# Performance work log

Measured on AMD Instinct MI355X. Metric: run time of the kernel, lower is better.

The kernel has to match this reference:

```python
import jax, jax.numpy as jnp
import numpy as np


def hard_sigmoid(v):
    # Keras 1.x default LSTM inner activation
    return jnp.clip(0.2 * v + 0.5, 0.0, 1.0)


def lstm_step(h, c, x_t, W, U, b):
    # Keras gate order: i, f, c(candidate), o
    z = x_t @ W + h @ U + b
    i, f, g, o = jnp.split(z, 4, axis=-1)
    i = hard_sigmoid(i)
    f = hard_sigmoid(f)
    g = jnp.tanh(g)
    o = hard_sigmoid(o)
    c_new = f * c + i * g
    h_new = o * jnp.tanh(c_new)
    return h_new, c_new


def setup_inputs() -> dict:
    key = jax.random.key(0)
    ks = jax.random.split(key, 8)
    B, L, D = 64, 1024, 512
    s = 0.05
    w = lambda k, shape: jax.random.normal(k, shape, jnp.float32) * s
    return {
        "x": jax.random.normal(ks[0], (B, L, D), jnp.float32),
        "Wr": w(ks[1], (D, 4 * D)),
        "Ur": w(ks[2], (D, 4 * D)),
        "br": jnp.zeros((4 * D,), jnp.float32),
        "Ww": w(ks[3], (D, 4 * D)),
        "Uw": w(ks[4], (D, 4 * D)),
        "bw": jnp.zeros((4 * D,), jnp.float32),
        "Wc": w(ks[5], (2 * D, D)),
        "bc": jnp.zeros((D,), jnp.float32),
    }


def reference(x, Wr, Ur, br, Ww, Uw, bw, Wc, bc):
    B, L, D = x.shape
    z0 = jnp.zeros((B, D), x.dtype)

    # --- reader LSTM over the full sequence (equation 1): o (L, B, D) ---
    def r_step(carry, x_t):
        h, c = carry
        h, c = lstm_step(h, c, x_t, Wr, Ur, br)
        return (h, c), h

    _, o_seq = jax.lax.scan(r_step, (z0, z0), jnp.swapaxes(x, 0, 1))

    # --- compose-and-write recurrence over memory (equations 2-6) ---
    mem0 = x  # mem_0 = input_to_read

    def w_step(carry, o_t):
        mem, hw, cw = carry                                   # mem: (B, L, D)
        z = jax.nn.softmax(jnp.einsum('bd,bld->bl', o_t, mem))  # attention over memory
        m_rt = jnp.einsum('bl,bld->bd', z, mem)                 # weighted read
        c_t = jnp.concatenate([o_t, m_rt], axis=-1) @ Wc + bc   # composer (linear)
        hw, cw = lstm_step(hw, cw, c_t, Ww, Uw, bw)             # writer LSTM step
        mem = mem * (1.0 - z[..., None]) + hw[:, None, :] * z[..., None]
        return (mem, hw, cw), None

    (mem_T, h_T, _), _ = jax.lax.scan(w_step, (mem0, z0, z0), o_seq)
    # return_mode == 'last_output'
    return h_T
```

## Files before the change

### kernel.cpp

```cpp
#include <hip/hip_runtime.h>
#include <math.h>

#define Bb 64
#define Ll 1024
#define Dd 512
#define G4 2048
#define KK 8
#define PART_STRIDE 524
#define WSL 12
#define RSL 8

__device__ __forceinline__ float hsig(float v){ return fminf(fmaxf(0.2f*v + 0.5f, 0.f), 1.f); }

__global__ __launch_bounds__(256) void wf_build(const float* __restrict__ Wc, const float* __restrict__ Ww,
                                                const float* __restrict__ Uw, float* __restrict__ Wf){
    const int k0 = (blockIdx.x >> 3) * 16;
    const int j  = (blockIdx.x & 7) * 256 + threadIdx.x;
    if (k0 < 2 * Dd){
        float acc[16];
        #pragma unroll
        for (int kk = 0; kk < 16; ++kk) acc[kk] = 0.f;
        for (int m = 0; m < Dd; ++m){
            float wv = Ww[(size_t)m * G4 + j];
            #pragma unroll
            for (int kk = 0; kk < 16; ++kk)
                acc[kk] = fmaf(Wc[(size_t)(k0 + kk) * Dd + m], wv, acc[kk]);
        }
        #pragma unroll
        for (int kk = 0; kk < 16; ++kk) Wf[(size_t)(k0 + kk) * G4 + j] = acc[kk];
    } else {
        #pragma unroll
        for (int kk = 0; kk < 16; ++kk)
            Wf[(size_t)(k0 + kk) * G4 + j] = Uw[(size_t)(k0 + kk - 2 * Dd) * G4 + j];
    }
}

__global__ __launch_bounds__(256) void bf_build(const float* __restrict__ bc, const float* __restrict__ Ww,
                                                const float* __restrict__ bw, float* __restrict__ bf){
    int j = blockIdx.x * 256 + threadIdx.x;
    float s = bw[j];
    for (int m = 0; m < Dd; ++m) s = fmaf(bc[m], Ww[(size_t)m * G4 + j], s);
    bf[j] = s;
}

__global__ __launch_bounds__(256) void gemm_reader(const float* __restrict__ xt, const float* __restrict__ h,
                                                   const float* __restrict__ Wr, const float* __restrict__ Ur,
                                                   float* __restrict__ part){
    __shared__ float inT[64][65];
    __shared__ float wT[64][32];
    const int bx = blockIdx.x;
    const int jt = bx & 63, ks = bx >> 6;
    const int j0 = jt * 32;
    const int k0 = ks * 256;
    const int tid = threadIdx.x;
    const int tj4 = (tid & 7) * 4;
    const int tb  = tid >> 3;
    float a00=0.f,a01=0.f,a02=0.f,a03=0.f;
    float a10=0.f,a11=0.f,a12=0.f,a13=0.f;
    for (int kk = 0; kk < 256; kk += 64){
        #pragma unroll
        for (int i = 0; i < 16; ++i){
            int idx = tid + i * 256;
            int b = idx >> 6, k = idx & 63;
            int kg = k0 + kk + k;
            inT[b][k] = (kg < Dd) ? xt[(size_t)b * (Ll * Dd) + kg] : h[b * Dd + kg - Dd];
        }
        #pragma unroll
        for (int i = 0; i < 8; ++i){
            int idx = tid + i * 256;
            int k = idx >> 5, j = idx & 31;
            int kg = k0 + kk + k;
            wT[k][j] = (kg < Dd) ? Wr[(size_t)kg * G4 + j0 + j] : Ur[(size_t)(kg - Dd) * G4 + j0 + j];
        }
        __syncthreads();
        #pragma unroll 8
        for (int k = 0; k < 64; ++k){
            float4 wv = *(const float4*)&wT[k][tj4];
            float i0 = inT[tb][k];
            float i1 = inT[tb + 32][k];
            a00 = fmaf(i0, wv.x, a00); a01 = fmaf(i0, wv.y, a01);
            a02 = fmaf(i0, wv.z, a02); a03 = fmaf(i0, wv.w, a03);
            a10 = fmaf(i1, wv.x, a10); a11 = fmaf(i1, wv.y, a11);
            a12 = fmaf(i1, wv.z, a12); a13 = fmaf(i1, wv.w, a13);
        }
        __syncthreads();
    }
    size_t o0 = (size_t)(ks * Bb + tb) * G4 + j0 + tj4;
    size_t o1 = (size_t)(ks * Bb + tb + 32) * G4 + j0 + tj4;
    *(float4*)&part[o0] = make_float4(a00, a01, a02, a03);
    *(float4*)&part[o1] = make_float4(a10, a11, a12, a13);
}

__global__ __launch_bounds__(256) void reader_pw(const float* __restrict__ part, const float* __restrict__ br,
                                                 float* __restrict__ h, float* __restrict__ c){
    int idx = blockIdx.x * 256 + threadIdx.x;
    int b = idx >> 9, d = idx & 511;
    float z[4];
    #pragma unroll
    for (int g = 0; g < 4; ++g){
        int j = g * Dd + d;
        float s = br[j];
        #pragma unroll
        for (int ks = 0; ks < 4; ++ks) s += part[(size_t)(ks * Bb + b) * G4 + j];
        z[g] = s;
    }
    float i = hsig(z[0]), f = hsig(z[1]), g2 = tanhf(z[2]), o = hsig(z[3]);
    float cn = fmaf(f, c[idx], i * g2);
    c[idx] = cn;
    h[idx] = o * tanhf(cn);
}

__global__ __launch_bounds__(256) void gemm_fast(const float* __restrict__ o, const float* __restrict__ mrt,
                                                 const float* __restrict__ hw, const float* __restrict__ Wf,
                                                 float* __restrict__ partW,
                                                 const float* __restrict__ xt1, const float* __restrict__ Wr,
                                                 const float* __restrict__ Ur, float* __restrict__ partR){
    __shared__ float inT[2][64][68];
    __shared__ float wT[2][64][36];
    const int bxg = blockIdx.x;
    const bool writer = (bxg < WSL * 64);
    const int bx = writer ? bxg : bxg - WSL * 64;
    const int jt = bx & 63;
    const int ks = bx >> 6;
    const int j0 = jt * 32;
    const int k0 = ks * 128;
    const int tid = threadIdx.x;
    const int tj4 = (tid & 7) * 4;
    const int tb  = tid >> 3;

    float4 aR0, aR1, aR2, aR3, wR0, wR1;
    auto LOAD = [&](int kk){
        #pragma unroll
        for (int i = 0; i < 4; ++i){
            int lin = tid + i * 256;
            int b = lin >> 4, k4 = (lin & 15) * 4;
            int kg = k0 + kk + k4;
            const float* src;
            if (writer){
                if (kg < Dd)           src = o   + b * Dd + kg;
                else if (kg < 2 * Dd)  src = mrt + b * Dd + kg - Dd;
                else                   src = hw  + b * Dd + kg - 2 * Dd;
            } else {
                src = (kg < Dd) ? xt1 + (size_t)b * (Ll * Dd) + kg
                                : o + b * Dd + kg - Dd;
            }
            float4 v = *(const float4*)src;
            if (i == 0) aR0 = v; else if (i == 1) aR1 = v; else if (i == 2) aR2 = v; else aR3 = v;
        }
        #pragma unroll
        for (int i = 0; i < 2; ++i){
            int lin = tid + i * 256;
            int k = lin >> 3, j4 = (lin & 7) * 4;
            int kg = k0 + kk + k;
            const float* src;
            if (writer) src = Wf + (size_t)kg * G4 + j0 + j4;
            else        src = (kg < Dd) ? Wr + (size_t)kg * G4 + j0 + j4
                                        : Ur + (size_t)(kg - Dd) * G4 + j0 + j4;
            float4 v = *(const float4*)src;
            if (i == 0) wR0 = v; else wR1 = v;
        }
    };
    auto STORE = [&](int buf){
        #pragma unroll
        for (int i = 0; i < 4; ++i){
            int lin = tid + i * 256;
            int b = lin >> 4, k4 = (lin & 15) * 4;
            float4 v = (i == 0) ? aR0 : (i == 1) ? aR1 : (i == 2) ? aR2 : aR3;
            *(float4*)&inT[buf][b][k4] = v;
        }
        #pragma unroll
        for (int i = 0; i < 2; ++i){
            int lin = tid + i * 256;
            int k = lin >> 3, j4 = (lin & 7) * 4;
            float4 v = (i == 0) ? wR0 : wR1;
            *(float4*)&wT[buf][k][j4] = v;
        }
    };

    float a00=0.f,a01=0.f,a02=0.f,a03=0.f;
    float a10=0.f,a11=0.f,a12=0.f,a13=0.f;

    LOAD(0);
    STORE(0);
    __syncthreads();
    LOAD(64);
    #pragma unroll 8
    for (int k = 0; k < 64; ++k){
        float4 wv = *(const float4*)&wT[0][k][tj4];
        float i0 = inT[0][tb][k];
        float i1 = inT[0][tb + 32][k];
        a00 = fmaf(i0, wv.x, a00); a01 = fmaf(i0, wv.y, a01);
        a02 = fmaf(i0, wv.z, a02); a03 = fmaf(i0, wv.w, a03);
        a10 = fmaf(i1, wv.x, a10); a11 = fmaf(i1, wv.y, a11);
        a12 = fmaf(i1, wv.z, a12); a13 = fmaf(i1, wv.w, a13);
    }
    STORE(1);
    __syncthreads();
    #pragma unroll 8
    for (int k = 0; k < 64; ++k){
        float4 wv = *(const float4*)&wT[1][k][tj4];
        float i0 = inT[1][tb][k];
        float i1 = inT[1][tb + 32][k];
        a00 = fmaf(i0, wv.x, a00); a01 = fmaf(i0, wv.y, a01);
        a02 = fmaf(i0, wv.z, a02); a03 = fmaf(i0, wv.w, a03);
        a10 = fmaf(i1, wv.x, a10); a11 = fmaf(i1, wv.y, a11);
        a12 = fmaf(i1, wv.z, a12); a13 = fmaf(i1, wv.w, a13);
    }
    float* part = writer ? partW : partR;
    size_t o0 = (size_t)(ks * Bb + tb) * G4 + j0 + tj4;
    size_t o1 = (size_t)(ks * Bb + tb + 32) * G4 + j0 + tj4;
    *(float4*)&part[o0] = make_float4(a00, a01, a02, a03);
    *(float4*)&part[o1] = make_float4(a10, a11, a12, a13);
}

__global__ __launch_bounds__(256) void pw_both(const float* __restrict__ partW, const float* __restrict__ bfv,
                                               float* __restrict__ hw, float* __restrict__ cw,
                                               float* __restrict__ out, int last,
                                               const float* __restrict__ partR, const float* __restrict__ br,
                                               float* __restrict__ h, float* __restrict__ c){
    const int bxg = blockIdx.x;
    const int writer = (bxg < 128) ? 1 : 0;
    const int idx = (writer ? bxg : bxg - 128) * 256 + threadIdx.x;
    const int b = idx >> 9, d = idx & 511;
    float z[4];
    #pragma unroll
    for (int g = 0; g < 4; ++g){
        int j = g * Dd + d;
        float s;
        if (writer){
            s = bfv[j];
            #pragma unroll
            for (int sl = 0; sl < WSL; ++sl) s += partW[(size_t)(sl * Bb + b) * G4 + j];
        } else {
            s = br[j];
            #pragma unroll
            for (int sl = 0; sl < RSL; ++sl) s += partR[(size_t)(sl * Bb + b) * G4 + j];
        }
        z[g] = s;
    }
    float i = hsig(z[0]), f = hsig(z[1]), g2 = tanhf(z[2]), o = hsig(z[3]);
    if (writer){
        float cn = fmaf(f, cw[idx], i * g2);
        cw[idx] = cn;
        float hn = o * tanhf(cn);
        hw[idx] = hn;
        if (last) out[idx] = hn;
    } else {
        float cn = fmaf(f, c[idx], i * g2);
        c[idx] = cn;
        h[idx] = o * tanhf(cn);
    }
}

__global__ __launch_bounds__(256, 4) void mega3(const float* memB, float* memOut,
                                                const float* __restrict__ o,
                                                float* __restrict__ scores, const float* __restrict__ Mb,
                                                const float* __restrict__ Sinv,
                                                float* __restrict__ part,
                                                float* __restrict__ Dv, float* __restrict__ Cv,
                                                const float* __restrict__ hwring,
                                                int mode, int p){
    __shared__ float DL[64];
    __shared__ float CORRL[64];
    __shared__ float CL[64][KK];
    __shared__ float GL[KK];
    __shared__ float HWL[KK][Dd];
    const int bid = blockIdx.x;
    const int b = bid >> 4, lb = bid & 15;
    const int tid = threadIdx.x;
    const int lane = tid & 63;
    const int wvi = tid >> 6;
    const int gw = lb * 4 + wvi;
    const int d0 = lane * 4, d1 = 256 + lane * 4;

    if (mode == 2){
        for (int ii = wvi; ii < p; ii += 4){
            const float* ov = o + b * Dd + lane * 8;
            const float* hv = hwring + ((size_t)ii * Bb + b) * Dd + lane * 8;
            float4 x0 = *(const float4*)ov;
            float4 x1 = *(const float4*)(ov + 4);
            float4 y0 = *(const float4*)hv;
            float4 y1 = *(const float4*)(hv + 4);
            float s = x0.x*y0.x + x0.y*y0.y + x0.z*y0.z + x0.w*y0.w
                    + x1.x*y1.x + x1.y*y1.y + x1.z*y1.z + x1.w*y1.w;
            #pragma unroll
            for (int off = 32; off; off >>= 1) s += __shfl_xor(s, off);
            if (lane == 0) GL[ii] = s;
        }
        __syncthreads();
    }

    if (mode){
        if (tid < 64){
            const int l = lb * 64 + tid;
            const size_t cbase = (size_t)(b * Ll + l) * KK;
            float z = __expf(scores[b * Ll + l] - Mb[b]) * Sinv[b];
            float om = 1.f - z;
            const int pm1 = (mode == 1) ? (KK - 1) : (p - 1);
            float cl[KK];
            float Dn;
            if (pm1 == 0){
                Dn = om;
                #pragma unroll
                for (int i = 0; i < KK; ++i) cl[i] = 0.f;
            } else {
                Dn = Dv[b * Ll + l] * om;
                #pragma unroll
                for (int i = 0; i < KK; ++i) cl[i] = Cv[cbase + i] * om;
                #pragma unroll
                for (int i = 0; i < KK; ++i) if (i > pm1) cl[i] = 0.f;
            }
            cl[pm1] = z;
            DL[tid] = Dn;
            #pragma unroll
            for (int i = 0; i < KK; ++i) CL[tid][i] = cl[i];
            if (mode == 2){
                Dv[b * Ll + l] = Dn;
                #pragma unroll
                for (int i = 0; i < KK; ++i) Cv[cbase + i] = cl[i];
                float corr = 0.f;
                #pragma unroll
                for (int i = 0; i < KK; ++i) corr = fmaf(cl[i], (i < p) ? GL[i] : 0.f, corr);
                CORRL[tid] = corr;
            }
        }
        if (mode == 1){
            for (int i = tid; i < KK * Dd; i += 256){
                int s = i >> 9, d = i & 511;
                HWL[s][d] = hwring[((size_t)s * Bb + b) * Dd + d];
            }
        }
        __syncthreads();
    }

    float4 oa  = *(const float4*)(o + b * Dd + d0);
    float4 obv = *(const float4*)(o + b * Dd + d1);
    const int lbase = gw * 16;
    float* srow = scores + b * Ll;

    float mA = -INFINITY, sAs = 0.f, mB = -INFINITY, sBs = 0.f;
    float A0x=0.f,A0y=0.f,A0z=0.f,A0w=0.f, A1x=0.f,A1y=0.f,A1z=0.f,A1w=0.f;
    float B0x=0.f,B0y=0.f,B0z=0.f,B0w=0.f, B1x=0.f,B1y=0.f,B1z=0.f,B1w=0.f;
    float my_s = 0.f;
    size_t baseA = ((size_t)b * Ll + lbase) * Dd;
    size_t baseB = baseA + (size_t)8 * Dd;

    if (mode == 1){
        #pragma unroll 2
        for (int r = 0; r < 8; ++r){
            const int locA = wvi * 16 + r, locB = locA + 8;
            float4 vA0 = *(const float4*)(memB + baseA + d0);
            float4 vA1 = *(const float4*)(memB + baseA + d1);
            float4 vB0 = *(const float4*)(memB + baseB + d0);
            float4 vB1 = *(const float4*)(memB + baseB + d1);
            float DnA = DL[locA], DnB = DL[locB];
            vA0.x *= DnA; vA0.y *= DnA; vA0.z *= DnA; vA0.w *= DnA;
            vA1.x *= DnA; vA1.y *= DnA; vA1.z *= DnA; vA1.w *= DnA;
            vB0.x *= DnB; vB0.y *= DnB; vB0.z *= DnB; vB0.w *= DnB;
            vB1.x *= DnB; vB1.y *= DnB; vB1.z *= DnB; vB1.w *= DnB;
            #pragma unroll
            for (int i = 0; i < KK; ++i){
                float cA = CL[locA][i], cB = CL[locB][i];
                float4 h0 = *(const float4*)&HWL[i][d0];
                float4 h1 = *(const float4*)&HWL[i][d1];
                vA0.x = fmaf(cA, h0.x, vA0.x); vA0.y = fmaf(cA, h0.y, vA0.y);
                vA0.z = fmaf(cA, h0.z, vA0.z); vA0.w = fmaf(cA, h0.w, vA0.w);
                vA1.x = fmaf(cA, h1.x, vA1.x); vA1.y = fmaf(cA, h1.y, vA1.y);
                vA1.z = fmaf(cA, h1.z, vA1.z); vA1.w = fmaf(cA, h1.w, vA1.w);
                vB0.x = fmaf(cB, h0.x, vB0.x); vB0.y = fmaf(cB, h0.y, vB0.y);
                vB0.z = fmaf(cB, h0.z, vB0.z); vB0.w = fmaf(cB, h0.w, vB0.w);
                vB1.x = fmaf(cB, h1.x, vB1.x); vB1.y = fmaf(cB, h1.y, vB1.y);
                vB1.z = fmaf(cB, h1.z, vB1.z); vB1.w = fmaf(cB, h1.w, vB1.w);
            }
            *(float4*)(memOut + baseA + d0) = vA0;
            *(float4*)(memOut + baseA + d1) = vA1;
            *(float4*)(memOut + baseB + d0) = vB0;
            *(float4*)(memOut + baseB + d1) = vB1;
            float sa = vA0.x*oa.x + vA0.y*oa.y + vA0.z*oa.z + vA0.w*oa.w
                     + vA1.x*obv.x + vA1.y*obv.y + vA1.z*obv.z + vA1.w*obv.w;
            float sb = vB0.x*oa.x + vB0.y*oa.y + vB0.z*oa.z + vB0.w*oa.w
                     + vB1.x*obv.x + vB1.y*obv.y + vB1.z*obv.z + vB1.w*obv.w;
            #pragma unroll
            for (int off = 32; off; off >>= 1){
                sa += __shfl_xor(sa, off);
                sb += __shfl_xor(sb, off);
            }
            if (lane == 0){ srow[lbase + r] = sa; srow[lbase + 8 + r] = sb; }
            float nmA = fmaxf(mA, sa);
            float scA = __expf(mA - nmA);
            float wtA = __expf(sa - nmA);
            sAs = fmaf(sAs, scA, wtA);
            A0x = fmaf(A0x, scA, vA0.x * wtA); A0y = fmaf(A0y, scA, vA0.y * wtA);
            A0z = fmaf(A0z, scA, vA0.z * wtA); A0w = fmaf(A0w, scA, vA0.w * wtA);
            A1x = fmaf(A1x, scA, vA1.x * wtA); A1y = fmaf(A1y, scA, vA1.y * wtA);
            A1z = fmaf(A1z, scA, vA1.z * wtA); A1w = fmaf(A1w, scA, vA1.w * wtA);
            mA = nmA;
            float nmB = fmaxf(mB, sb);
            float scB = __expf(mB - nmB);
            float wtB = __expf(sb - nmB);
            sBs = fmaf(sBs, scB, wtB);
            B0x = fmaf(B0x, scB, vB0.x * wtB); B0y = fmaf(B0y, scB, vB0.y * wtB);
            B0z = fmaf(B0z, scB, vB0.z * wtB); B0w = fmaf(B0w, scB, vB0.w * wtB);
            B1x = fmaf(B1x, scB, vB1.x * wtB); B1y = fmaf(B1y, scB, vB1.y * wtB);
            B1z = fmaf(B1z, scB, vB1.z * wtB); B1w = fmaf(B1w, scB, vB1.w * wtB);
            mB = nmB;
            baseA += Dd; baseB += Dd;
        }
    } else {
        #pragma unroll 2
        for (int r = 0; r < 8; ++r){
            const int locA = wvi * 16 + r, locB = locA + 8;
            float4 vA0 = *(const float4*)(memB + baseA + d0);
            float4 vA1 = *(const float4*)(memB + baseA + d1);
            float4 vB0 = *(const float4*)(memB + baseB + d0);
            float4 vB1 = *(const float4*)(memB + baseB + d1);
            float sa = vA0.x*oa.x + vA0.y*oa.y + vA0.z*oa.z + vA0.w*oa.w
                     + vA1.x*obv.x + vA1.y*obv.y + vA1.z*obv.z + vA1.w*obv.w;
            float sb = vB0.x*oa.x + vB0.y*oa.y + vB0.z*oa.z + vB0.w*oa.w
                     + vB1.x*obv.x + vB1.y*obv.y + vB1.z*obv.z + vB1.w*obv.w;
            #pragma unroll
            for (int off = 32; off; off >>= 1){
                sa += __shfl_xor(sa, off);
                sb += __shfl_xor(sb, off);
            }
            float DnA = 1.f, DnB = 1.f;
            if (mode == 2){
                DnA = DL[locA]; DnB = DL[locB];
                sa = fmaf(DnA, sa, CORRL[locA]);
                sb = fmaf(DnB, sb, CORRL[locB]);
            }
            if (lane == 0){ srow[lbase + r] = sa; srow[lbase + 8 + r] = sb; }
            if (lane == r)     my_s = sa;
            if (lane == 8 + r) my_s = sb;
            float nmA = fmaxf(mA, sa);
            float scA = __expf(mA - nmA);
            float wtA = __expf(sa - nmA);
            float wdA = wtA * DnA;
            sAs = fmaf(sAs, scA, wtA);
            A0x = fmaf(A0x, scA, vA0.x * wdA); A0y = fmaf(A0y, scA, vA0.y * wdA);
            A0z = fmaf(A0z, scA, vA0.z * wdA); A0w = fmaf(A0w, scA, vA0.w * wdA);
            A1x = fmaf(A1x, scA, vA1.x * wdA); A1y = fmaf(A1y, scA, vA1.y * wdA);
            A1z = fmaf(A1z, scA, vA1.z * wdA); A1w = fmaf(A1w, scA, vA1.w * wdA);
            mA = nmA;
            float nmB = fmaxf(mB, sb);
            float scB = __expf(mB - nmB);
            float wtB = __expf(sb - nmB);
            float wdB = wtB * DnB;
            sBs = fmaf(sBs, scB, wtB);
            B0x = fmaf(B0x, scB, vB0.x * wdB); B0y = fmaf(B0y, scB, vB0.y * wdB);
            B0z = fmaf(B0z, scB, vB0.z * wdB); B0w = fmaf(B0w, scB, vB0.w * wdB);
            B1x = fmaf(B1x, scB, vB1.x * wdB); B1y = fmaf(B1y, scB, vB1.y * wdB);
            B1z = fmaf(B1z, scB, vB1.z * wdB); B1w = fmaf(B1w, scB, vB1.w * wdB);
            mB = nmB;
            baseA += Dd; baseB += Dd;
        }
    }
    float M = fmaxf(mA, mB);
    float eA = __expf(mA - M), eB = __expf(mB - M);
    float ssum = sAs * eA + sBs * eB;
    float* pp = part + (size_t)(b * 64 + gw) * PART_STRIDE;
    *(float4*)(pp + d0) = make_float4(A0x * eA + B0x * eB, A0y * eA + B0y * eB,
                                      A0z * eA + B0z * eB, A0w * eA + B0w * eB);
    *(float4*)(pp + d1) = make_float4(A1x * eA + B1x * eB, A1y * eA + B1y * eB,
                                      A1z * eA + B1z * eB, A1w * eA + B1w * eB);
    if (lane == 0){ pp[512] = M; pp[513] = ssum; }
    if (mode == 2){
        float wexp = (lane < 16) ? __expf(my_s - M) : 0.f;
        float gacc = 0.f;
        const int ci = lane & 7;
        #pragma unroll
        for (int l = 0; l < 16; ++l){
            float wl = __shfl(wexp, l);
            gacc = fmaf(wl, CL[wvi * 16 + l][ci], gacc);
        }
        if (lane < 8) pp[514 + lane] = gacc;
    }
}

__global__ __launch_bounds__(256) void small_a(const float* __restrict__ part, float* __restrict__ mrt,
                                               float* __restrict__ Mb, float* __restrict__ Sinv,
                                               const float* __restrict__ hwring, int p){
    const int b = blockIdx.x >> 2, dseg = blockIdx.x & 3;
    const int tid = threadIdx.x;
    __shared__ float ews[64];
    __shared__ float psum[256];
    __shared__ float gam[KK][8];
    if (tid < 64){
        const float* pp = part + (size_t)(b * 64 + tid) * PART_STRIDE;
        float mw = pp[512], sw = pp[513];
        float M = mw;
        #pragma unroll
        for (int off = 32; off; off >>= 1) M = fmaxf(M, __shfl_xor(M, off));
        float e = __expf(mw - M);
        float Ssum = sw * e;
        #pragma unroll
        for (int off = 32; off; off >>= 1) Ssum += __shfl_xor(Ssum, off);
        float Si = 1.f / Ssum;
        ews[tid] = e * Si;
        if (dseg == 0 && tid == 0){ Mb[b] = M; Sinv[b] = Si; }
    }
    __syncthreads();
    if (p > 0 && tid < 64){
        const int i = tid & 7, ch = tid >> 3;
        float s = 0.f;
        #pragma unroll
        for (int w2 = 0; w2 < 8; ++w2)
            s = fmaf(part[(size_t)(b * 64 + ch * 8 + w2) * PART_STRIDE + 514 + i], ews[ch * 8 + w2], s);
        gam[i][ch] = s;
    }
    __syncthreads();
    if (p > 0 && tid < 8){
        float s = gam[tid][0];
        #pragma unroll
        for (int ch = 1; ch < 8; ++ch) s += gam[tid][ch];
        gam[tid][0] = s;
    }
    const int dl = tid & 127, half = tid >> 7;
    const int d = dseg * 128 + dl;
    const float* pb = part + (size_t)(b * 64 + half * 32) * PART_STRIDE + d;
    float s = 0.f;
    #pragma unroll 8
    for (int w2 = 0; w2 < 32; ++w2)
        s = fmaf(pb[(size_t)w2 * PART_STRIDE], ews[half * 32 + w2], s);
    psum[tid] = s;
    __syncthreads();
    if (half == 0){
        float r = psum[tid] + psum[tid + 128];
        for (int i = 0; i < p; ++i)
            r = fmaf(gam[i][0], hwring[((size_t)i * Bb + b) * Dd + d], r);
        mrt[b * Dd + d] = r;
    }
}

extern "C" void kernel_launch(void* const* d_in, const int* in_sizes, int n_in,
                              void* d_out, int out_size, void* d_ws, size_t ws_size,
                              hipStream_t stream) {
    (void)in_sizes; (void)n_in; (void)out_size;
    const float* x  = (const float*)d_in[0];
    const float* Wr = (const float*)d_in[1];
    const float* Ur = (const float*)d_in[2];
    const float* br = (const float*)d_in[3];
    const float* Ww = (const float*)d_in[4];
    const float* Uw = (const float*)d_in[5];
    const float* bw = (const float*)d_in[6];
    const float* Wc = (const float*)d_in[7];
    const float* bc = (const float*)d_in[8];
    float* out = (float*)d_out;

    float* w = (float*)d_ws;
    float* mem     = w; w += (size_t)Bb * Ll * Dd;
    float* scores  = w; w += (size_t)Bb * Ll;
    float* part_me = w; w += (size_t)Bb * 64 * PART_STRIDE;
    float* Mb      = w; w += 64;
    float* Sinv    = w; w += 64;
    float* mrt     = w; w += (size_t)Bb * Dd;
    float* Dv      = w; w += (size_t)Bb * Ll;
    float* Cv      = w; w += (size_t)Bb * Ll * KK;
    float* h_r     = w; w += (size_t)Bb * Dd;
    float* c_r     = w; w += (size_t)Bb * Dd;
    float* cw      = w; w += (size_t)Bb * Dd;
    float* hwring  = w; w += (size_t)KK * Bb * Dd;
    float* partR   = w; w += (size_t)RSL * Bb * G4;
    float* partW   = w; w += (size_t)WSL * Bb * G4;
    float* Wf      = w; w += (size_t)1536 * G4;
    float* bf      = w; w += G4;
    size_t need = (size_t)(w - (float*)d_ws) * sizeof(float);
    if (ws_size < need) return;

    hipMemsetAsync(h_r, 0, (size_t)(3 + KK) * Bb * Dd * sizeof(float), stream);
    wf_build<<<(1536 / 16) * 8, 256, 0, stream>>>(Wc, Ww, Uw, Wf);
    bf_build<<<G4 / 256, 256, 0, stream>>>(bc, Ww, bw, bf);

    gemm_reader<<<256, 256, 0, stream>>>(x, h_r, Wr, Ur, partR);
    reader_pw<<<128, 256, 0, stream>>>(partR, br, h_r, c_r);

    for (int t = 0; t < Ll; ++t){
        const int p = t & (KK - 1);
        const int mode = (t == 0) ? 0 : ((p == 0) ? 1 : 2);
        const float* mi = (t <= KK) ? x : mem;
        mega3<<<1024, 256, 0, stream>>>(mi, mem, h_r, scores, Mb, Sinv, part_me,
                                        Dv, Cv, hwring, mode, p);
        small_a<<<256, 256, 0, stream>>>(part_me, mrt, Mb, Sinv, hwring, (mode == 2) ? p : 0);
        int tn = (t + 1 < Ll) ? t + 1 : t;
        const float* hwprev = hwring + ((size_t)((t + KK - 1) & (KK - 1)) * Bb) * Dd;
        gemm_fast<<<(WSL + RSL) * 64, 256, 0, stream>>>(h_r, mrt, hwprev, Wf, partW,
                                                        x + (size_t)tn * Dd, Wr, Ur, partR);
        float* hwnew = hwring + ((size_t)(t & (KK - 1)) * Bb) * Dd;
        pw_both<<<256, 256, 0, stream>>>(partW, bf, hwnew, cw, out, t == Ll - 1 ? 1 : 0,
                                         partR, br, h_r, c_r);
    }
}
```

Measured before the change: 68.69 ms.

## Double lazy memory-update window and split attention kernel into factor and materialize variants

Raises the deferred low-rank memory update window from 8 to 16 steps, so the full memory tensor is rewritten half as often. The monolithic attention kernel becomes two specialised kernels: one that materialises the memory update and one that works from the factored form, which removes mode branches and the large shared hw buffer from the common path. The trade-off is more correction coefficients per row, larger Cv/part buffers, and a 32 KB shared tile in the materialising kernel, which may lower occupancy there.

```diff
diff --git a/kernel.cpp b/kernel.cpp
--- a/kernel.cpp
+++ b/kernel.cpp
@@ -5,8 +5,8 @@
 #define Ll 1024
 #define Dd 512
 #define G4 2048
-#define KK 8
-#define PART_STRIDE 524
+#define KK 16
+#define PART_STRIDE 532
 #define WSL 12
 #define RSL 8
 
@@ -252,19 +252,18 @@
     }
 }
 
-__global__ __launch_bounds__(256, 4) void mega3(const float* memB, float* memOut,
-                                                const float* __restrict__ o,
-                                                float* __restrict__ scores, const float* __restrict__ Mb,
-                                                const float* __restrict__ Sinv,
-                                                float* __restrict__ part,
-                                                float* __restrict__ Dv, float* __restrict__ Cv,
-                                                const float* __restrict__ hwring,
-                                                int mode, int p){
+__global__ __launch_bounds__(256, 4) void mega_factor(const float* __restrict__ memB,
+                                                      const float* __restrict__ o,
+                                                      float* __restrict__ scores, const float* __restrict__ Mb,
+                                                      const float* __restrict__ Sinv,
+                                                      float* __restrict__ part,
+                                                      float* __restrict__ Dv, float* __restrict__ Cv,
+                                                      const float* __restrict__ hwring,
+                                                      int mode, int p){
     __shared__ float DL[64];
     __shared__ float CORRL[64];
     __shared__ float CL[64][KK];
     __shared__ float GL[KK];
-    __shared__ float HWL[KK][Dd];
     const int bid = blockIdx.x;
     const int b = bid >> 4, lb = bid & 15;
     const int tid = threadIdx.x;
@@ -288,15 +287,13 @@
             if (lane == 0) GL[ii] = s;
         }
         __syncthreads();
-    }
-
-    if (mode){
+
         if (tid < 64){
             const int l = lb * 64 + tid;
             const size_t cbase = (size_t)(b * Ll + l) * KK;
             float z = __expf(scores[b * Ll + l] - Mb[b]) * Sinv[b];
             float om = 1.f - z;
-            const int pm1 = (mode == 1) ? (KK - 1) : (p - 1);
+            const int pm1 = p - 1;
             float cl[KK];
             float Dn;
             if (pm1 == 0){
@@ -314,21 +311,13 @@
             DL[tid] = Dn;
             #pragma unroll
             for (int i = 0; i < KK; ++i) CL[tid][i] = cl[i];
-            if (mode == 2){
-                Dv[b * Ll + l] = Dn;
-                #pragma unroll
-                for (int i = 0; i < KK; ++i) Cv[cbase + i] = cl[i];
-                float corr = 0.f;
-                #pragma unroll
-                for (int i = 0; i < KK; ++i) corr = fmaf(cl[i], (i < p) ? GL[i] : 0.f, corr);
-                CORRL[tid] = corr;
-            }
-        }
-        if (mode == 1){
-            for (int i = tid; i < KK * Dd; i += 256){
-                int s = i >> 9, d = i & 511;
-                HWL[s][d] = hwring[((size_t)s * Bb + b) * Dd + d];
-            }
+            Dv[b * Ll + l] = Dn;
+            #pragma unroll
+            for (int i = 0; i < KK; ++i) Cv[cbase + i] = cl[i];
+            float corr = 0.f;
+            #pragma unroll
+            for (int i = 0; i < KK; ++i) corr = fmaf(cl[i], (i < p) ? GL[i] : 0.f, corr);
+            CORRL[tid] = corr;
         }
         __syncthreads();
     }
@@ -345,115 +334,52 @@
     size_t baseA = ((size_t)b * Ll + lbase) * Dd;
     size_t baseB = baseA + (size_t)8 * Dd;
 
-    if (mode == 1){
-        #pragma unroll 2
-        for (int r = 0; r < 8; ++r){
-            const int locA = wvi * 16 + r, locB = locA + 8;
-            float4 vA0 = *(const float4*)(memB + baseA + d0);
-            float4 vA1 = *(const float4*)(memB + baseA + d1);
-            float4 vB0 = *(const float4*)(memB + baseB + d0);
-            float4 vB1 = *(const float4*)(memB + baseB + d1);
-            float DnA = DL[locA], DnB = DL[locB];
-            vA0.x *= DnA; vA0.y *= DnA; vA0.z *= DnA; vA0.w *= DnA;
-            vA1.x *= DnA; vA1.y *= DnA; vA1.z *= DnA; vA1.w *= DnA;
-            vB0.x *= DnB; vB0.y *= DnB; vB0.z *= DnB; vB0.w *= DnB;
-            vB1.x *= DnB; vB1.y *= DnB; vB1.z *= DnB; vB1.w *= DnB;
-            #pragma unroll
-            for (int i = 0; i < KK; ++i){
-                float cA = CL[locA][i], cB = CL[locB][i];
-                float4 h0 = *(const float4*)&HWL[i][d0];
-                float4 h1 = *(const float4*)&HWL[i][d1];
-                vA0.x = fmaf(cA, h0.x, vA0.x); vA0.y = fmaf(cA, h0.y, vA0.y);
-                vA0.z = fmaf(cA, h0.z, vA0.z); vA0.w = fmaf(cA, h0.w, vA0.w);
-                vA1.x = fmaf(cA, h1.x, vA1.x); vA1.y = fmaf(cA, h1.y, vA1.y);
-                vA1.z = fmaf(cA, h1.z, vA1.z); vA1.w = fmaf(cA, h1.w, vA1.w);
-                vB0.x = fmaf(cB, h0.x, vB0.x); vB0.y = fmaf(cB, h0.y, vB0.y);
-                vB0.z = fmaf(cB, h0.z, vB0.z); vB0.w = fmaf(cB, h0.w, vB0.w);
-                vB1.x = fmaf(cB, h1.x, vB1.x); vB1.y = fmaf(cB, h1.y, vB1.y);
-                vB1.z = fmaf(cB, h1.z, vB1.z); vB1.w = fmaf(cB, h1.w, vB1.w);
-            }
-            *(float4*)(memOut + baseA + d0) = vA0;
-            *(float4*)(memOut + baseA + d1) = vA1;
-            *(float4*)(memOut + baseB + d0) = vB0;
-            *(float4*)(memOut + baseB + d1) = vB1;
-            float sa = vA0.x*oa.x + vA0.y*oa.y + vA0.z*oa.z + vA0.w*oa.w
-                     + vA1.x*obv.x + vA1.y*obv.y + vA1.z*obv.z + vA1.w*obv.w;
-            float sb = vB0.x*oa.x + vB0.y*oa.y + vB0.z*oa.z + vB0.w*oa.w
-                     + vB1.x*obv.x + vB1.y*obv.y + vB1.z*obv.z + vB1.w*obv.w;
-            #pragma unroll
-            for (int off = 32; off; off >>= 1){
-                sa += __shfl_xor(sa, off);
-                sb += __shfl_xor(sb, off);
-            }
-            if (lane == 0){ srow[lbase + r] = sa; srow[lbase + 8 + r] = sb; }
-            float nmA = fmaxf(mA, sa);
-            float scA = __expf(mA - nmA);
-            float wtA = __expf(sa - nmA);
-            sAs = fmaf(sAs, scA, wtA);
-            A0x = fmaf(A0x, scA, vA0.x * wtA); A0y = fmaf(A0y, scA, vA0.y * wtA);
-            A0z = fmaf(A0z, scA, vA0.z * wtA); A0w = fmaf(A0w, scA, vA0.w * wtA);
-            A1x = fmaf(A1x, scA, vA1.x * wtA); A1y = fmaf(A1y, scA, vA1.y * wtA);
-            A1z = fmaf(A1z, scA, vA1.z * wtA); A1w = fmaf(A1w, scA, vA1.w * wtA);
-            mA = nmA;
-            float nmB = fmaxf(mB, sb);
-            float scB = __expf(mB - nmB);
-            float wtB = __expf(sb - nmB);
-            sBs = fmaf(sBs, scB, wtB);
-            B0x = fmaf(B0x, scB, vB0.x * wtB); B0y = fmaf(B0y, scB, vB0.y * wtB);
-            B0z = fmaf(B0z, scB, vB0.z * wtB); B0w = fmaf(B0w, scB, vB0.w * wtB);
-            B1x = fmaf(B1x, scB, vB1.x * wtB); B1y = fmaf(B1y, scB, vB1.y * wtB);
-            B1z = fmaf(B1z, scB, vB1.z * wtB); B1w = fmaf(B1w, scB, vB1.w * wtB);
-            mB = nmB;
-            baseA += Dd; baseB += Dd;
-        }
-    } else {
-        #pragma unroll 2
-        for (int r = 0; r < 8; ++r){
-            const int locA = wvi * 16 + r, locB = locA + 8;
-            float4 vA0 = *(const float4*)(memB + baseA + d0);
-            float4 vA1 = *(const float4*)(memB + baseA + d1);
-            float4 vB0 = *(const float4*)(memB + baseB + d0);
-            float4 vB1 = *(const float4*)(memB + baseB + d1);
-            float sa = vA0.x*oa.x + vA0.y*oa.y + vA0.z*oa.z + vA0.w*oa.w
-                     + vA1.x*obv.x + vA1.y*obv.y + vA1.z*obv.z + vA1.w*obv.w;
-            float sb = vB0.x*oa.x + vB0.y*oa.y + vB0.z*oa.z + vB0.w*oa.w
-                     + vB1.x*obv.x + vB1.y*obv.y + vB1.z*obv.z + vB1.w*obv.w;
-            #pragma unroll
-            for (int off = 32; off; off >>= 1){
-                sa += __shfl_xor(sa, off);
-                sb += __shfl_xor(sb, off);
-            }
-            float DnA = 1.f, DnB = 1.f;
-            if (mode == 2){
-                DnA = DL[locA]; DnB = DL[locB];
-                sa = fmaf(DnA, sa, CORRL[locA]);
-                sb = fmaf(DnB, sb, CORRL[locB]);
-            }
-            if (lane == 0){ srow[lbase + r] = sa; srow[lbase + 8 + r] = sb; }
-            if (lane == r)     my_s = sa;
-            if (lane == 8 + r) my_s = sb;
-            float nmA = fmaxf(mA, sa);
-            float scA = __expf(mA - nmA);
-            float wtA = __expf(sa - nmA);
-            float wdA = wtA * DnA;
-            sAs = fmaf(sAs, scA, wtA);
-            A0x = fmaf(A0x, scA, vA0.x * wdA); A0y = fmaf(A0y, scA, vA0.y * wdA);
-            A0z = fmaf(A0z, scA, vA0.z * wdA); A0w = fmaf(A0w, scA, vA0.w * wdA);
-            A1x = fmaf(A1x, scA, vA1.x * wdA); A1y = fmaf(A1y, scA, vA1.y * wdA);
-            A1z = fmaf(A1z, scA, vA1.z * wdA); A1w = fmaf(A1w, scA, vA1.w * wdA);
-            mA = nmA;
-            float nmB = fmaxf(mB, sb);
-            float scB = __expf(mB - nmB);
-            float wtB = __expf(sb - nmB);
-            float wdB = wtB * DnB;
-            sBs = fmaf(sBs, scB, wtB);
-            B0x = fmaf(B0x, scB, vB0.x * wdB); B0y = fmaf(B0y, scB, vB0.y * wdB);
-            B0z = fmaf(B0z, scB, vB0.z * wdB); B0w = fmaf(B0w, scB, vB0.w * wdB);
-            B1x = fmaf(B1x, scB, vB1.x * wdB); B1y = fmaf(B1y, scB, vB1.y * wdB);
-            B1z = fmaf(B1z, scB, vB1.z * wdB); B1w = fmaf(B1w, scB, vB1.w * wdB);
-            mB = nmB;
-            baseA += Dd; baseB += Dd;
-        }
+    #pragma unroll 2
+    for (int r = 0; r < 8; ++r){
+        const int locA = wvi * 16 + r, locB = locA + 8;
+        float4 vA0 = *(const float4*)(memB + baseA + d0);
+        float4 vA1 = *(const float4*)(memB + baseA + d1);
+        float4 vB0 = *(const float4*)(memB + baseB + d0);
+        float4 vB1 = *(const float4*)(memB + baseB + d1);
+        float sa = vA0.x*oa.x + vA0.y*oa.y + vA0.z*oa.z + vA0.w*oa.w
+                 + vA1.x*obv.x + vA1.y*obv.y + vA1.z*obv.z + vA1.w*obv.w;
+        float sb = vB0.x*oa.x + vB0.y*oa.y + vB0.z*oa.z + vB0.w*oa.w
+                 + vB1.x*obv.x + vB1.y*obv.y + vB1.z*obv.z + vB1.w*obv.w;
+        #pragma unroll
+        for (int off = 32; off; off >>= 1){
+            sa += __shfl_xor(sa, off);
+            sb += __shfl_xor(sb, off);
+        }
+        float DnA = 1.f, DnB = 1.f;
+        if (mode == 2){
+            DnA = DL[locA]; DnB = DL[locB];
+            sa = fmaf(DnA, sa, CORRL[locA]);
+            sb = fmaf(DnB, sb, CORRL[locB]);
+        }
+        if (lane == 0){ srow[lbase + r] = sa; srow[lbase + 8 + r] = sb; }
+        if (lane == r)     my_s = sa;
+        if (lane == 8 + r) my_s = sb;
+        float nmA = fmaxf(mA, sa);
+        float scA = __expf(mA - nmA);
+        float wtA = __expf(sa - nmA);
+        float wdA = wtA * DnA;
+        sAs = fmaf(sAs, scA, wtA);
+        A0x = fmaf(A0x, scA, vA0.x * wdA); A0y = fmaf(A0y, scA, vA0.y * wdA);
+        A0z = fmaf(A0z, scA, vA0.z * wdA); A0w = fmaf(A0w, scA, vA0.w * wdA);
+        A1x = fmaf(A1x, scA, vA1.x * wdA); A1y = fmaf(A1y, scA, vA1.y * wdA);
+        A1z = fmaf(A1z, scA, vA1.z * wdA); A1w = fmaf(A1w, scA, vA1.w * wdA);
+        mA = nmA;
+        float nmB = fmaxf(mB, sb);
+        float scB = __expf(mB - nmB);
+        float wtB = __expf(sb - nmB);
+        float wdB = wtB * DnB;
+        sBs = fmaf(sBs, scB, wtB);
+        B0x = fmaf(B0x, scB, vB0.x * wdB); B0y = fmaf(B0y, scB, vB0.y * wdB);
+        B0z = fmaf(B0z, scB, vB0.z * wdB); B0w = fmaf(B0w, scB, vB0.w * wdB);
+        B1x = fmaf(B1x, scB, vB1.x * wdB); B1y = fmaf(B1y, scB, vB1.y * wdB);
+        B1z = fmaf(B1z, scB, vB1.z * wdB); B1w = fmaf(B1w, scB, vB1.w * wdB);
+        mB = nmB;
+        baseA += Dd; baseB += Dd;
     }
     float M = fmaxf(mA, mB);
     float eA = __expf(mA - M), eB = __expf(mB - M);
@@ -467,14 +393,134 @@
     if (mode == 2){
         float wexp = (lane < 16) ? __expf(my_s - M) : 0.f;
         float gacc = 0.f;
-        const int ci = lane & 7;
+        const int ci = lane & 15;
         #pragma unroll
         for (int l = 0; l < 16; ++l){
             float wl = __shfl(wexp, l);
             gacc = fmaf(wl, CL[wvi * 16 + l][ci], gacc);
         }
-        if (lane < 8) pp[514 + lane] = gacc;
-    }
+        if (lane < 16) pp[514 + lane] = gacc;
+    }
+}
+
+__global__ __launch_bounds__(256, 4) void mega_mat(const float* __restrict__ memB, float* __restrict__ memOut,
+                                                   const float* __restrict__ o,
+                                                   float* __restrict__ scores, const float* __restrict__ Mb,
+                                                   const float* __restrict__ Sinv,
+                                                   float* __restrict__ part,
+                                                   const float* __restrict__ Dv, const float* __restrict__ Cv,
+                                                   const float* __restrict__ hwring){
+    __shared__ float DL[64];
+    __shared__ float CL[64][KK];
+    __shared__ float HWL[KK][Dd];
+    const int bid = blockIdx.x;
+    const int b = bid >> 4, lb = bid & 15;
+    const int tid = threadIdx.x;
+    const int lane = tid & 63;
+    const int wvi = tid >> 6;
+    const int gw = lb * 4 + wvi;
+    const int d0 = lane * 4, d1 = 256 + lane * 4;
+
+    if (tid < 64){
+        const int l = lb * 64 + tid;
+        const size_t cbase = (size_t)(b * Ll + l) * KK;
+        float z = __expf(scores[b * Ll + l] - Mb[b]) * Sinv[b];
+        float om = 1.f - z;
+        float cl[KK];
+        float Dn = Dv[b * Ll + l] * om;
+        #pragma unroll
+        for (int i = 0; i < KK; ++i) cl[i] = Cv[cbase + i] * om;
+        cl[KK - 1] = z;
+        DL[tid] = Dn;
+        #pragma unroll
+        for (int i = 0; i < KK; ++i) CL[tid][i] = cl[i];
+    }
+    for (int i = tid; i < KK * Dd; i += 256){
+        int s = i >> 9, d = i & 511;
+        HWL[s][d] = hwring[((size_t)s * Bb + b) * Dd + d];
+    }
+    __syncthreads();
+
+    float4 oa  = *(const float4*)(o + b * Dd + d0);
+    float4 obv = *(const float4*)(o + b * Dd + d1);
+    const int lbase = gw * 16;
+    float* srow = scores + b * Ll;
+
+    float mA = -INFINITY, sAs = 0.f, mB = -INFINITY, sBs = 0.f;
+    float A0x=0.f,A0y=0.f,A0z=0.f,A0w=0.f, A1x=0.f,A1y=0.f,A1z=0.f,A1w=0.f;
+    float B0x=0.f,B0y=0.f,B0z=0.f,B0w=0.f, B1x=0.f,B1y=0.f,B1z=0.f,B1w=0.f;
+    size_t baseA = ((size_t)b * Ll + lbase) * Dd;
+    size_t baseB = baseA + (size_t)8 * Dd;
+
+    #pragma unroll 2
+    for (int r = 0; r < 8; ++r){
+        const int locA = wvi * 16 + r, locB = locA + 8;
+        float4 vA0 = *(const float4*)(memB + baseA + d0);
+        float4 vA1 = *(const float4*)(memB + baseA + d1);
+        float4 vB0 = *(const float4*)(memB + baseB + d0);
+        float4 vB1 = *(const float4*)(memB + baseB + d1);
+        float DnA = DL[locA], DnB = DL[locB];
+        vA0.x *= DnA; vA0.y *= DnA; vA0.z *= DnA; vA0.w *= DnA;
+        vA1.x *= DnA; vA1.y *= DnA; vA1.z *= DnA; vA1.w *= DnA;
+        vB0.x *= DnB; vB0.y *= DnB; vB0.z *= DnB; vB0.w *= DnB;
+        vB1.x *= DnB; vB1.y *= DnB; vB1.z *= DnB; vB1.w *= DnB;
+        #pragma unroll
+        for (int i = 0; i < KK; ++i){
+            float cA = CL[locA][i], cB = CL[locB][i];
+            float4 h0 = *(const float4*)&HWL[i][d0];
+            float4 h1 = *(const float4*)&HWL[i][d1];
+            vA0.x = fmaf(cA, h0.x, vA0.x); vA0.y = fmaf(cA, h0.y, vA0.y);
+            vA0.z = fmaf(cA, h0.z, vA0.z); vA0.w = fmaf(cA, h0.w, vA0.w);
+            vA1.x = fmaf(cA, h1.x, vA1.x); vA1.y = fmaf(cA, h1.y, vA1.y);
+            vA1.z = fmaf(cA, h1.z, vA1.z); vA1.w = fmaf(cA, h1.w, vA1.w);
+            vB0.x = fmaf(cB, h0.x, vB0.x); vB0.y = fmaf(cB, h0.y, vB0.y);
+            vB0.z = fmaf(cB, h0.z, vB0.z); vB0.w = fmaf(cB, h0.w, vB0.w);
+            vB1.x = fmaf(cB, h1.x, vB1.x); vB1.y = fmaf(cB, h1.y, vB1.y);
+            vB1.z = fmaf(cB, h1.z, vB1.z); vB1.w = fmaf(cB, h1.w, vB1.w);
+        }
+        *(float4*)(memOut + baseA + d0) = vA0;
+        *(float4*)(memOut + baseA + d1) = vA1;
+        *(float4*)(memOut + baseB + d0) = vB0;
+        *(float4*)(memOut + baseB + d1) = vB1;
+        float sa = vA0.x*oa.x + vA0.y*oa.y + vA0.z*oa.z + vA0.w*oa.w
+                 + vA1.x*obv.x + vA1.y*obv.y + vA1.z*obv.z + vA1.w*obv.w;
+        float sb = vB0.x*oa.x + vB0.y*oa.y + vB0.z*oa.z + vB0.w*oa.w
+                 + vB1.x*obv.x + vB1.y*obv.y + vB1.z*obv.z + vB1.w*obv.w;
+        #pragma unroll
+        for (int off = 32; off; off >>= 1){
+            sa += __shfl_xor(sa, off);
+            sb += __shfl_xor(sb, off);
+        }
+        if (lane == 0){ srow[lbase + r] = sa; srow[lbase + 8 + r] = sb; }
+        float nmA = fmaxf(mA, sa);
+        float scA = __expf(mA - nmA);
+        float wtA = __expf(sa - nmA);
+        sAs = fmaf(sAs, scA, wtA);
+        A0x = fmaf(A0x, scA, vA0.x * wtA); A0y = fmaf(A0y, scA, vA0.y * wtA);
+        A0z = fmaf(A0z, scA, vA0.z * wtA); A0w = fmaf(A0w, scA, vA0.w * wtA);
+        A1x = fmaf(A1x, scA, vA1.x * wtA); A1y = fmaf(A1y, scA, vA1.y * wtA);
+        A1z = fmaf(A1z, scA, vA1.z * wtA); A1w = fmaf(A1w, scA, vA1.w * wtA);
+        mA = nmA;
+        float nmB = fmaxf(mB, sb);
+        float scB = __expf(mB - nmB);
+        float wtB = __expf(sb - nmB);
+        sBs = fmaf(sBs, scB, wtB);
+        B0x = fmaf(B0x, scB, vB0.x * wtB); B0y = fmaf(B0y, scB, vB0.y * wtB);
+        B0z = fmaf(B0z, scB, vB0.z * wtB); B0w = fmaf(B0w, scB, vB0.w * wtB);
+        B1x = fmaf(B1x, scB, vB1.x * wtB); B1y = fmaf(B1y, scB, vB1.y * wtB);
+        B1z = fmaf(B1z, scB, vB1.z * wtB); B1w = fmaf(B1w, scB, vB1.w * wtB);
+        mB = nmB;
+        baseA += Dd; baseB += Dd;
+    }
+    float M = fmaxf(mA, mB);
+    float eA = __expf(mA - M), eB = __expf(mB - M);
+    float ssum = sAs * eA + sBs * eB;
+    float* pp = part + (size_t)(b * 64 + gw) * PART_STRIDE;
+    *(float4*)(pp + d0) = make_float4(A0x * eA + B0x * eB, A0y * eA + B0y * eB,
+                                      A0z * eA + B0z * eB, A0w * eA + B0w * eB);
+    *(float4*)(pp + d1) = make_float4(A1x * eA + B1x * eB, A1y * eA + B1y * eB,
+                                      A1z * eA + B1z * eB, A1w * eA + B1w * eB);
+    if (lane == 0){ pp[512] = M; pp[513] = ssum; }
 }
 
 __global__ __launch_bounds__(256) void small_a(const float* __restrict__ part, float* __restrict__ mrt,
@@ -500,8 +546,8 @@
         if (dseg == 0 && tid == 0){ Mb[b] = M; Sinv[b] = Si; }
     }
     __syncthreads();
-    if (p > 0 && tid < 64){
-        const int i = tid & 7, ch = tid >> 3;
+    if (p > 0 && tid < 128){
+        const int i = tid & 15, ch = tid >> 4;
         float s = 0.f;
         #pragma unroll
         for (int w2 = 0; w2 < 8; ++w2)
@@ -509,7 +555,7 @@
         gam[i][ch] = s;
     }
     __syncthreads();
-    if (p > 0 && tid < 8){
+    if (p > 0 && tid < 16){
         float s = gam[tid][0];
         #pragma unroll
         for (int ch = 1; ch < 8; ++ch) s += gam[tid][ch];
@@ -578,8 +624,12 @@
         const int p = t & (KK - 1);
         const int mode = (t == 0) ? 0 : ((p == 0) ? 1 : 2);
         const float* mi = (t <= KK) ? x : mem;
-        mega3<<<1024, 256, 0, stream>>>(mi, mem, h_r, scores, Mb, Sinv, part_me,
-                                        Dv, Cv, hwring, mode, p);
+        if (mode == 1)
+            mega_mat<<<1024, 256, 0, stream>>>(mi, mem, h_r, scores, Mb, Sinv, part_me,
+                                               Dv, Cv, hwring);
+        else
+            mega_factor<<<1024, 256, 0, stream>>>(mi, h_r, scores, Mb, Sinv, part_me,
+                                                  Dv, Cv, hwring, mode, p);
         small_a<<<256, 256, 0, stream>>>(part_me, mrt, Mb, Sinv, hwring, (mode == 2) ? p : 0);
         int tn = (t + 1 < Ll) ? t + 1 : t;
         const float* hwprev = hwring + ((size_t)((t + KK - 1) & (KK - 1)) * Bb) * Dd;
```

Result: slower. 80.06 ms (+16.6%).
